# Kernel optimization log

Hardware: AMD Instinct MI355X
Metric: run time of the kernel (lower is better)

## Reference

```python
import jax, jax.numpy as jnp
import numpy as np

EPS = 1e-8
RESOLUTION = 32
DILATION = 1


def _stencils(resolution=RESOLUTION, dilation=DILATION):
    # interior grid of resolution^2 samples in [-1, 1]^2 (cell centers)
    lin = (np.arange(resolution) + 0.5) / resolution * 2.0 - 1.0
    gy, gx = np.meshgrid(lin, lin, indexing='ij')
    inner = np.stack([gy.ravel(), gx.ravel()], -1).astype(np.float32)
    # perimeter ring dilated outward by `dilation` cells
    scale = (resolution + 2.0 * dilation) / resolution
    mask = np.zeros((resolution, resolution), bool)
    mask[0, :] = mask[-1, :] = mask[:, 0] = mask[:, -1] = True
    outer = (inner[mask.ravel()] * scale).astype(np.float32)
    # append homogeneous coordinate (matches torch.concat with ones)
    s_in = np.concatenate([inner, np.ones((inner.shape[0], 1), np.float32)], -1)
    s_out = np.concatenate([outer, np.ones((outer.shape[0], 1), np.float32)], -1)
    return jnp.asarray(s_in), jnp.asarray(s_out)


def _bilinear(image, pos):
    # image: (H, W); pos: (..., 2) pixel coords (row, col); clamped bilinear
    H, W = image.shape
    i = pos[..., 0]
    j = pos[..., 1]
    i0 = jnp.clip(jnp.floor(i), 0, H - 2).astype(jnp.int32)
    j0 = jnp.clip(jnp.floor(j), 0, W - 2).astype(jnp.int32)
    di = jnp.clip(i - i0, 0.0, 1.0)
    dj = jnp.clip(j - j0, 0.0, 1.0)
    v00 = image[i0, j0]
    v01 = image[i0, j0 + 1]
    v10 = image[i0 + 1, j0]
    v11 = image[i0 + 1, j0 + 1]
    return (v00 * (1 - di) * (1 - dj) + v01 * (1 - di) * dj
            + v10 * di * (1 - dj) + v11 * di * dj)


def setup_inputs() -> dict:
    key = jax.random.key(0)
    k1, k2 = jax.random.split(key)
    S, P = 4, 4096
    H = W = 2048
    u = jax.random.uniform(k1, (S, P, 5), dtype=jnp.float32)
    xy = u[..., :2] * (H - 1)              # centers inside the image
    ab = 4.0 + u[..., 2:4] * 20.0          # half extents in [4, 24] px
    th = u[..., 4:5] * jnp.float32(np.pi)  # angle in [0, pi)
    points = jnp.concatenate([xy, ab, th], axis=-1)
    points_mask = jnp.ones((S, P), dtype=jnp.float32)
    position_energy_map = jax.random.normal(k2, (1, H, W), dtype=jnp.float32)
    stencil_in, stencil_out = _stencils()
    return {"points": points, "points_mask": points_mask,
            "position_energy_map": position_energy_map,
            "stencil_in": stencil_in, "stencil_out": stencil_out}


def reference(points, points_mask, position_energy_map, stencil_in, stencil_out):
    # affine_from_state: (x, y, a, b, theta) -> 2x3 affine, shape (S, P, 2, 3)
    x, y = points[..., 0], points[..., 1]
    a, b = points[..., 2], points[..., 3]
    t = points[..., 4]
    c, s = jnp.cos(t), jnp.sin(t)
    A = jnp.stack([jnp.stack([a * c, -b * s, x], -1),
                   jnp.stack([a * s, b * c, y], -1)], -2)
    # stencil coordinates in image space: (S, P, n_stencil, 2)
    coords_in = jnp.einsum('spij,nj->spni', A, stencil_in)
    coords_out = jnp.einsum('spij,nj->spni', A, stencil_out)
    img = position_energy_map[0]
    in_values = _bilinear(img, coords_in)    # (S, P, n_in)
    out_values = _bilinear(img, coords_out)  # (S, P, n_out)
    # contrast_measure: t-test-like contrast along stencil dim
    m_in, m_out = in_values.mean(-1), out_values.mean(-1)
    v_in = in_values.var(-1, ddof=1)
    v_out = out_values.var(-1, ddof=1)
    contrast = (m_in - m_out) / jnp.sqrt(v_in + v_out + EPS)
    return contrast * points_mask
```

## Files before the change

### kernel.cpp

```cpp
#include <hip/hip_runtime.h>
#include <math.h>

__global__ __launch_bounds__(256) void contrast_kernel_fast(
    const float* __restrict__ points,
    const float* __restrict__ mask,
    const float* __restrict__ img,
    float* __restrict__ out,
    int n_points)
{
    constexpr int W = 2048;
    constexpr int H = 2048;
    constexpr float fImax = (float)(H - 2);
    constexpr float fJmax = (float)(W - 2);

    const int wave = (int)((blockIdx.x * (unsigned)blockDim.x + threadIdx.x) >> 6);
    const int lane = (int)(threadIdx.x & 63u);
    if (wave >= n_points) return;

    const float* pt = points + (size_t)wave * 5;
    const float px = pt[0];
    const float py = pt[1];
    const float a  = pt[2];
    const float b  = pt[3];
    const float th = pt[4];

    float sn, cs;
    sincosf(th, &sn, &cs);
    const float A00 = a * cs, A01 = -b * sn;
    const float A10 = a * sn, A11 =  b * cs;

    const float sx = fmaf((float)(lane & 31), 0.0625f, 0.03125f) - 1.0f;
    const int   hi = lane >> 5;
    const float bi = fmaf(A01, sx, px);
    const float bj = fmaf(A11, sx, py);

    float s0 = 0.f, q0 = 0.f, s1 = 0.f, q1 = 0.f;
    #pragma unroll
    for (int it = 0; it < 16; ++it) {
        const float sy = fmaf((float)(2 * it + hi), 0.0625f, 0.03125f) - 1.0f;
        const float ci = fmaf(A00, sy, bi);
        const float cj = fmaf(A10, sy, bj);
        const float fi = fminf(fmaxf(floorf(ci), 0.f), fImax);
        const float fj = fminf(fmaxf(floorf(cj), 0.f), fJmax);
        const float di = fminf(fmaxf(ci - fi, 0.f), 1.f);
        const float dj = fminf(fmaxf(cj - fj, 0.f), 1.f);
        const float* p0 = img + (((int)fi << 11) + (int)fj);
        float2 r0, r1;
        __builtin_memcpy(&r0, p0, sizeof(float2));
        __builtin_memcpy(&r1, p0 + W, sizeof(float2));
        const float top = fmaf(r0.y - r0.x, dj, r0.x);
        const float bot = fmaf(r1.y - r1.x, dj, r1.x);
        const float v   = fmaf(bot - top, di, top);
        if (it & 1) { s1 += v; q1 = fmaf(v, v, q1); }
        else        { s0 += v; q0 = fmaf(v, v, q0); }
    }
    float sum_in = s0 + s1;
    float sq_in  = q0 + q1;

    float sum_out = 0.f, sq_out = 0.f;
    #pragma unroll
    for (int base = 0; base < 124; base += 64) {
        const int n = base + lane;
        if (n < 124) {
            int row, col;
            if (n < 32)      { row = 0;                 col = n; }
            else if (n < 92) { row = 1 + ((n - 32) >> 1); col = (n & 1) * 31; }
            else             { row = 31;                col = n - 92; }
            const float sy = (fmaf((float)row, 0.0625f, 0.03125f) - 1.0f) * 1.0625f;
            const float sxo = (fmaf((float)col, 0.0625f, 0.03125f) - 1.0f) * 1.0625f;
            const float ci = fmaf(A00, sy, fmaf(A01, sxo, px));
            const float cj = fmaf(A10, sy, fmaf(A11, sxo, py));
            const float fi = fminf(fmaxf(floorf(ci), 0.f), fImax);
            const float fj = fminf(fmaxf(floorf(cj), 0.f), fJmax);
            const float di = fminf(fmaxf(ci - fi, 0.f), 1.f);
            const float dj = fminf(fmaxf(cj - fj, 0.f), 1.f);
            const float* p0 = img + (((int)fi << 11) + (int)fj);
            float2 r0, r1;
            __builtin_memcpy(&r0, p0, sizeof(float2));
            __builtin_memcpy(&r1, p0 + W, sizeof(float2));
            const float top = fmaf(r0.y - r0.x, dj, r0.x);
            const float bot = fmaf(r1.y - r1.x, dj, r1.x);
            const float v   = fmaf(bot - top, di, top);
            sum_out += v;
            sq_out = fmaf(v, v, sq_out);
        }
    }

    #pragma unroll
    for (int off = 32; off > 0; off >>= 1) {
        sum_in  += __shfl_xor(sum_in,  off);
        sq_in   += __shfl_xor(sq_in,   off);
        sum_out += __shfl_xor(sum_out, off);
        sq_out  += __shfl_xor(sq_out,  off);
    }

    if (lane == 0) {
        const float ni = 1024.f, no = 124.f;
        const float m_in  = sum_in  / ni;
        const float m_out = sum_out / no;
        const float v_in  = (sq_in  - ni * m_in  * m_in ) / (ni - 1.f);
        const float v_out = (sq_out - no * m_out * m_out) / (no - 1.f);
        const float contrast = (m_in - m_out) / sqrtf(v_in + v_out + 1e-8f);
        out[wave] = contrast * mask[wave];
    }
}

__global__ __launch_bounds__(256) void contrast_kernel_generic(
    const float* __restrict__ points, const float* __restrict__ mask,
    const float* __restrict__ img, const float* __restrict__ st_in,
    const float* __restrict__ st_out, float* __restrict__ out,
    int n_points, int n_in, int n_out, int Himg, int Wimg)
{
    const int wave = (int)((blockIdx.x * (unsigned)blockDim.x + threadIdx.x) >> 6);
    const int lane = (int)(threadIdx.x & 63u);
    if (wave >= n_points) return;
    const float* pt = points + (size_t)wave * 5;
    const float px = pt[0], py = pt[1], a = pt[2], b = pt[3], th = pt[4];
    float sn, cs; sincosf(th, &sn, &cs);
    const float A00 = a * cs, A01 = -b * sn, A10 = a * sn, A11 = b * cs;
    const float fImax = (float)(Himg - 2), fJmax = (float)(Wimg - 2);
    float sum_in = 0.f, sq_in = 0.f;
    for (int base = 0; base < n_in; base += 64) {
        const int n = base + lane;
        if (n < n_in) {
            const float sy = st_in[n * 3 + 0], sx = st_in[n * 3 + 1];
            const float ci = fmaf(A00, sy, fmaf(A01, sx, px));
            const float cj = fmaf(A10, sy, fmaf(A11, sx, py));
            const float fi = fminf(fmaxf(floorf(ci), 0.f), fImax);
            const float fj = fminf(fmaxf(floorf(cj), 0.f), fJmax);
            const float di = fminf(fmaxf(ci - fi, 0.f), 1.f);
            const float dj = fminf(fmaxf(cj - fj, 0.f), 1.f);
            const float* p0 = img + ((int)fi * Wimg + (int)fj);
            const float v00 = p0[0], v01 = p0[1], v10 = p0[Wimg], v11 = p0[Wimg + 1];
            const float top = fmaf(v01 - v00, dj, v00);
            const float bot = fmaf(v11 - v10, dj, v10);
            const float v = fmaf(bot - top, di, top);
            sum_in += v; sq_in = fmaf(v, v, sq_in);
        }
    }
    float sum_out = 0.f, sq_out = 0.f;
    for (int base = 0; base < n_out; base += 64) {
        const int n = base + lane;
        if (n < n_out) {
            const float sy = st_out[n * 3 + 0], sx = st_out[n * 3 + 1];
            const float ci = fmaf(A00, sy, fmaf(A01, sx, px));
            const float cj = fmaf(A10, sy, fmaf(A11, sx, py));
            const float fi = fminf(fmaxf(floorf(ci), 0.f), fImax);
            const float fj = fminf(fmaxf(floorf(cj), 0.f), fJmax);
            const float di = fminf(fmaxf(ci - fi, 0.f), 1.f);
            const float dj = fminf(fmaxf(cj - fj, 0.f), 1.f);
            const float* p0 = img + ((int)fi * Wimg + (int)fj);
            const float v00 = p0[0], v01 = p0[1], v10 = p0[Wimg], v11 = p0[Wimg + 1];
            const float top = fmaf(v01 - v00, dj, v00);
            const float bot = fmaf(v11 - v10, dj, v10);
            const float v = fmaf(bot - top, di, top);
            sum_out += v; sq_out = fmaf(v, v, sq_out);
        }
    }
    #pragma unroll
    for (int off = 32; off > 0; off >>= 1) {
        sum_in += __shfl_xor(sum_in, off);  sq_in += __shfl_xor(sq_in, off);
        sum_out += __shfl_xor(sum_out, off); sq_out += __shfl_xor(sq_out, off);
    }
    if (lane == 0) {
        const float ni = (float)n_in, no = (float)n_out;
        const float m_in = sum_in / ni, m_out = sum_out / no;
        const float v_in = (sq_in - ni * m_in * m_in) / (ni - 1.f);
        const float v_out = (sq_out - no * m_out * m_out) / (no - 1.f);
        const float contrast = (m_in - m_out) / sqrtf(v_in + v_out + 1e-8f);
        out[wave] = contrast * mask[wave];
    }
}

extern "C" void kernel_launch(void* const* d_in, const int* in_sizes, int n_in_bufs,
                              void* d_out, int out_size, void* d_ws, size_t ws_size,
                              hipStream_t stream) {
    (void)n_in_bufs; (void)d_ws; (void)ws_size; (void)out_size;
    const float* points = (const float*)d_in[0];
    const float* mask   = (const float*)d_in[1];
    const float* img    = (const float*)d_in[2];
    const float* st_in  = (const float*)d_in[3];
    const float* st_out = (const float*)d_in[4];
    float* out = (float*)d_out;

    const int n_points = in_sizes[0] / 5;
    const int n_in     = in_sizes[3] / 3;
    const int n_out    = in_sizes[4] / 3;
    const int hw       = in_sizes[2];

    const int waves_per_block = 4;
    const int blocks = (n_points + waves_per_block - 1) / waves_per_block;

    if (n_in == 1024 && n_out == 124 && hw == 2048 * 2048) {
        contrast_kernel_fast<<<blocks, 256, 0, stream>>>(points, mask, img, out, n_points);
    } else {
        int Wimg = 1;
        while ((long long)Wimg * Wimg < (long long)hw) Wimg <<= 1;
        const int Himg = hw / Wimg;
        contrast_kernel_generic<<<blocks, 256, 0, stream>>>(points, mask, img, st_in, st_out,
                                                            out, n_points, n_in, n_out, Himg, Wimg);
    }
}
```

Measured before the change: 116.6 us.

## Split each point across two waves with 8x8 tiled stencil sampling

Each point is now handled by two waves in a block instead of one, so the block covers two points. Each wave samples half of the 1024 inner stencil points and half of the 124 outer ones, and the two partial sums are combined through shared memory after a __syncthreads. Inner samples are assigned in 8x8 spatial tiles rather than 32-wide rows, so the gather addresses of one instruction are more compact in the image. The aim is more waves in flight to hide gather latency and better cache-line reuse, at the cost of a block-level barrier and duplicated per-point setup such as sincos.

```diff
diff --git a/kernel.cpp b/kernel.cpp
--- a/kernel.cpp
+++ b/kernel.cpp
@@ -13,11 +13,15 @@
     constexpr float fImax = (float)(H - 2);
     constexpr float fJmax = (float)(W - 2);
 
-    const int wave = (int)((blockIdx.x * (unsigned)blockDim.x + threadIdx.x) >> 6);
+    __shared__ float partial[4][4];
+
+    const int wib  = (int)(threadIdx.x >> 6);
     const int lane = (int)(threadIdx.x & 63u);
-    if (wave >= n_points) return;
-
-    const float* pt = points + (size_t)wave * 5;
+    const int pid  = blockIdx.x * 2 + (wib >> 1);
+    const int half = wib & 1;
+    if (pid >= n_points) return;
+
+    const float* pt = points + (size_t)pid * 5;
     const float px = pt[0];
     const float py = pt[1];
     const float a  = pt[2];
@@ -29,17 +33,23 @@
     const float A00 = a * cs, A01 = -b * sn;
     const float A10 = a * sn, A11 =  b * cs;
 
-    const float sx = fmaf((float)(lane & 31), 0.0625f, 0.03125f) - 1.0f;
-    const int   hi = lane >> 5;
-    const float bi = fmaf(A01, sx, px);
-    const float bj = fmaf(A11, sx, py);
+    const int r8 = lane >> 3;
+    const int c8 = lane & 7;
+    const float sy0 = fmaf((float)r8, 0.0625f, 0.03125f) - 1.0f;
+    const float sx0 = fmaf((float)c8, 0.0625f, 0.03125f) - 1.0f;
+    const float ci0 = fmaf(A00, sy0, fmaf(A01, sx0, px));
+    const float cj0 = fmaf(A10, sy0, fmaf(A11, sx0, py));
+    const float A00h = A00 * 0.5f, A01h = A01 * 0.5f;
+    const float A10h = A10 * 0.5f, A11h = A11 * 0.5f;
 
     float s0 = 0.f, q0 = 0.f, s1 = 0.f, q1 = 0.f;
     #pragma unroll
-    for (int it = 0; it < 16; ++it) {
-        const float sy = fmaf((float)(2 * it + hi), 0.0625f, 0.03125f) - 1.0f;
-        const float ci = fmaf(A00, sy, bi);
-        const float cj = fmaf(A10, sy, bj);
+    for (int t = 0; t < 8; ++t) {
+        const int tile = half * 8 + t;
+        const float ftr = (float)(tile >> 2);
+        const float ftc = (float)(tile & 3);
+        const float ci = fmaf(A00h, ftr, fmaf(A01h, ftc, ci0));
+        const float cj = fmaf(A10h, ftr, fmaf(A11h, ftc, cj0));
         const float fi = fminf(fmaxf(floorf(ci), 0.f), fImax);
         const float fj = fminf(fmaxf(floorf(cj), 0.f), fJmax);
         const float di = fminf(fmaxf(ci - fi, 0.f), 1.f);
@@ -51,25 +61,24 @@
         const float top = fmaf(r0.y - r0.x, dj, r0.x);
         const float bot = fmaf(r1.y - r1.x, dj, r1.x);
         const float v   = fmaf(bot - top, di, top);
-        if (it & 1) { s1 += v; q1 = fmaf(v, v, q1); }
-        else        { s0 += v; q0 = fmaf(v, v, q0); }
+        if (t & 1) { s1 += v; q1 = fmaf(v, v, q1); }
+        else       { s0 += v; q0 = fmaf(v, v, q0); }
     }
     float sum_in = s0 + s1;
     float sq_in  = q0 + q1;
 
     float sum_out = 0.f, sq_out = 0.f;
-    #pragma unroll
-    for (int base = 0; base < 124; base += 64) {
-        const int n = base + lane;
-        if (n < 124) {
+    {
+        const int n = half * 62 + lane;
+        if (lane < 62) {
             int row, col;
-            if (n < 32)      { row = 0;                 col = n; }
+            if (n < 32)      { row = 0;                   col = n; }
             else if (n < 92) { row = 1 + ((n - 32) >> 1); col = (n & 1) * 31; }
-            else             { row = 31;                col = n - 92; }
+            else             { row = 31;                  col = n - 92; }
             const float sy = (fmaf((float)row, 0.0625f, 0.03125f) - 1.0f) * 1.0625f;
-            const float sxo = (fmaf((float)col, 0.0625f, 0.03125f) - 1.0f) * 1.0625f;
-            const float ci = fmaf(A00, sy, fmaf(A01, sxo, px));
-            const float cj = fmaf(A10, sy, fmaf(A11, sxo, py));
+            const float sx = (fmaf((float)col, 0.0625f, 0.03125f) - 1.0f) * 1.0625f;
+            const float ci = fmaf(A00, sy, fmaf(A01, sx, px));
+            const float cj = fmaf(A10, sy, fmaf(A11, sx, py));
             const float fi = fminf(fmaxf(floorf(ci), 0.f), fImax);
             const float fj = fminf(fmaxf(floorf(cj), 0.f), fJmax);
             const float di = fminf(fmaxf(ci - fi, 0.f), 1.f);
@@ -81,8 +90,8 @@
             const float top = fmaf(r0.y - r0.x, dj, r0.x);
             const float bot = fmaf(r1.y - r1.x, dj, r1.x);
             const float v   = fmaf(bot - top, di, top);
-            sum_out += v;
-            sq_out = fmaf(v, v, sq_out);
+            sum_out = v;
+            sq_out  = v * v;
         }
     }
 
@@ -95,13 +104,25 @@
     }
 
     if (lane == 0) {
+        partial[wib][0] = sum_in;
+        partial[wib][1] = sq_in;
+        partial[wib][2] = sum_out;
+        partial[wib][3] = sq_out;
+    }
+    __syncthreads();
+
+    if (lane == 0 && half == 0) {
+        const float S_in  = partial[wib][0] + partial[wib + 1][0];
+        const float Q_in  = partial[wib][1] + partial[wib + 1][1];
+        const float S_out = partial[wib][2] + partial[wib + 1][2];
+        const float Q_out = partial[wib][3] + partial[wib + 1][3];
         const float ni = 1024.f, no = 124.f;
-        const float m_in  = sum_in  / ni;
-        const float m_out = sum_out / no;
-        const float v_in  = (sq_in  - ni * m_in  * m_in ) / (ni - 1.f);
-        const float v_out = (sq_out - no * m_out * m_out) / (no - 1.f);
+        const float m_in  = S_in  / ni;
+        const float m_out = S_out / no;
+        const float v_in  = (Q_in  - ni * m_in  * m_in ) / (ni - 1.f);
+        const float v_out = (Q_out - no * m_out * m_out) / (no - 1.f);
         const float contrast = (m_in - m_out) / sqrtf(v_in + v_out + 1e-8f);
-        out[wave] = contrast * mask[wave];
+        out[pid] = contrast * mask[pid];
     }
 }
 
@@ -188,15 +209,14 @@
     const int n_out    = in_sizes[4] / 3;
     const int hw       = in_sizes[2];
 
-    const int waves_per_block = 4;
-    const int blocks = (n_points + waves_per_block - 1) / waves_per_block;
-
     if (n_in == 1024 && n_out == 124 && hw == 2048 * 2048) {
+        const int blocks = (n_points + 1) / 2;
         contrast_kernel_fast<<<blocks, 256, 0, stream>>>(points, mask, img, out, n_points);
     } else {
         int Wimg = 1;
         while ((long long)Wimg * Wimg < (long long)hw) Wimg <<= 1;
         const int Himg = hw / Wimg;
+        const int blocks = (n_points + 3) / 4;
         contrast_kernel_generic<<<blocks, 256, 0, stream>>>(points, mask, img, st_in, st_out,
                                                             out, n_points, n_in, n_out, Himg, Wimg);
     }
```

Result: no change. 118.7 us (+1.8%).

## Convert image to padded fp16 workspace and skip clamping for interior ellipses

Applied to the files above, without the earlier changes.

Adds a pre-pass that converts the fp32 energy map to fp16 with a padded row stride in the workspace, so the main kernel gathers half-size data with fewer cache misses. The main kernel picks an unclamped tap path when the ellipse's bounding box lies inside the image, and switches the inner loop from full unroll to unroll 2. The cost is an extra full-image conversion pass every call and fp16 rounding of the image values, which changes numerical accuracy.

```diff
diff --git a/kernel.cpp b/kernel.cpp
--- a/kernel.cpp
+++ b/kernel.cpp
@@ -1,18 +1,106 @@
 #include <hip/hip_runtime.h>
+#include <hip/hip_fp16.h>
 #include <math.h>
 
-__global__ __launch_bounds__(256) void contrast_kernel_fast(
+
+#define PSTRIDE 2080
+
+__global__ __launch_bounds__(256) void convert_img_f16_pad(
+    const float4* __restrict__ src, __half* __restrict__ dst)
+{
+    const int row = (int)blockIdx.x;
+    const int t   = (int)threadIdx.x;
+    const float4 a = src[(size_t)row * 512 + t * 2];
+    const float4 b = src[(size_t)row * 512 + t * 2 + 1];
+    union { __half2 h[4]; uint4 u; } o;
+    o.h[0] = __float22half2_rn(make_float2(a.x, a.y));
+    o.h[1] = __float22half2_rn(make_float2(a.z, a.w));
+    o.h[2] = __float22half2_rn(make_float2(b.x, b.y));
+    o.h[3] = __float22half2_rn(make_float2(b.z, b.w));
+    *(uint4*)(dst + (size_t)row * PSTRIDE + t * 8) = o.u;
+}
+
+template<bool CLAMP>
+__device__ __forceinline__ float tap_pad(const __half* __restrict__ img,
+                                         float ci, float cj)
+{
+    float fi = floorf(ci), fj = floorf(cj);
+    if (CLAMP) {
+        fi = fminf(fmaxf(fi, 0.f), 2046.f);
+        fj = fminf(fmaxf(fj, 0.f), 2046.f);
+    }
+    float di = ci - fi, dj = cj - fj;
+    if (CLAMP) {
+        di = fminf(fmaxf(di, 0.f), 1.f);
+        dj = fminf(fmaxf(dj, 0.f), 1.f);
+    }
+    const int r = (int)fi, c = (int)fj;
+    const int base = (r << 11) + (r << 5) + c;
+    const int even = base & ~1;
+    const int sh   = (base & 1) << 4;
+    uint2 q0, q1;
+    __builtin_memcpy(&q0, img + even, 8);
+    __builtin_memcpy(&q1, img + even + PSTRIDE, 8);
+    const unsigned p0 = (unsigned)((((unsigned long long)q0.y << 32) | q0.x) >> sh);
+    const unsigned p1 = (unsigned)((((unsigned long long)q1.y << 32) | q1.x) >> sh);
+    const float2 f0 = __half22float2(*reinterpret_cast<const __half2*>(&p0));
+    const float2 f1 = __half22float2(*reinterpret_cast<const __half2*>(&p1));
+    const float top = fmaf(f0.y - f0.x, dj, f0.x);
+    const float bot = fmaf(f1.y - f1.x, dj, f1.x);
+    return fmaf(bot - top, di, top);
+}
+
+template<bool CLAMP>
+__device__ __forceinline__ void accum_pad(
+    const __half* __restrict__ img, int lane,
+    float A00, float A01, float A10, float A11, float px, float py,
+    float& sum_in, float& sq_in, float& sum_out, float& sq_out)
+{
+    const float sx = fmaf((float)(lane & 31), 0.0625f, 0.03125f) - 1.0f;
+    const int   hi = lane >> 5;
+    const float bi = fmaf(A01, sx, px);
+    const float bj = fmaf(A11, sx, py);
+
+    float s0 = 0.f, q0 = 0.f, s1 = 0.f, q1 = 0.f;
+    #pragma unroll 2
+    for (int it = 0; it < 16; ++it) {
+        const float sy = fmaf((float)(2 * it + hi), 0.0625f, 0.03125f) - 1.0f;
+        const float ci = fmaf(A00, sy, bi);
+        const float cj = fmaf(A10, sy, bj);
+        const float v  = tap_pad<CLAMP>(img, ci, cj);
+        if (it & 1) { s1 += v; q1 = fmaf(v, v, q1); }
+        else        { s0 += v; q0 = fmaf(v, v, q0); }
+    }
+    sum_in = s0 + s1;
+    sq_in  = q0 + q1;
+
+    sum_out = 0.f; sq_out = 0.f;
+    #pragma unroll
+    for (int base = 0; base < 124; base += 64) {
+        const int n = base + lane;
+        if (n < 124) {
+            int row, col;
+            if (n < 32)      { row = 0;                   col = n; }
+            else if (n < 92) { row = 1 + ((n - 32) >> 1); col = (n & 1) * 31; }
+            else             { row = 31;                  col = n - 92; }
+            const float sy = (fmaf((float)row, 0.0625f, 0.03125f) - 1.0f) * 1.0625f;
+            const float sxo = (fmaf((float)col, 0.0625f, 0.03125f) - 1.0f) * 1.0625f;
+            const float ci = fmaf(A00, sy, fmaf(A01, sxo, px));
+            const float cj = fmaf(A10, sy, fmaf(A11, sxo, py));
+            const float v  = tap_pad<CLAMP>(img, ci, cj);
+            sum_out += v;
+            sq_out = fmaf(v, v, sq_out);
+        }
+    }
+}
+
+__global__ __launch_bounds__(256, 8) void contrast_f16_pad(
     const float* __restrict__ points,
     const float* __restrict__ mask,
-    const float* __restrict__ img,
+    const __half* __restrict__ img,
     float* __restrict__ out,
     int n_points)
 {
-    constexpr int W = 2048;
-    constexpr int H = 2048;
-    constexpr float fImax = (float)(H - 2);
-    constexpr float fJmax = (float)(W - 2);
-
     const int wave = (int)((blockIdx.x * (unsigned)blockDim.x + threadIdx.x) >> 6);
     const int lane = (int)(threadIdx.x & 63u);
     if (wave >= n_points) return;
@@ -29,13 +117,58 @@
     const float A00 = a * cs, A01 = -b * sn;
     const float A10 = a * sn, A11 =  b * cs;
 
+    const float Ri = (fabsf(A00) + fabsf(A01)) * 1.04f;
+    const float Rj = (fabsf(A10) + fabsf(A11)) * 1.04f;
+    const bool interior = (px >= Ri + 0.5f) && (px <= 2046.0f - Ri) &&
+                          (py >= Rj + 0.5f) && (py <= 2046.0f - Rj);
+
+    float sum_in, sq_in, sum_out, sq_out;
+    if (interior) {
+        accum_pad<false>(img, lane, A00, A01, A10, A11, px, py,
+                         sum_in, sq_in, sum_out, sq_out);
+    } else {
+        accum_pad<true>(img, lane, A00, A01, A10, A11, px, py,
+                        sum_in, sq_in, sum_out, sq_out);
+    }
+
+    #pragma unroll
+    for (int off = 32; off > 0; off >>= 1) {
+        sum_in  += __shfl_xor(sum_in,  off);
+        sq_in   += __shfl_xor(sq_in,   off);
+        sum_out += __shfl_xor(sum_out, off);
+        sq_out  += __shfl_xor(sq_out,  off);
+    }
+
+    if (lane == 0) {
+        const float ni = 1024.f, no = 124.f;
+        const float m_in  = sum_in  / ni;
+        const float m_out = sum_out / no;
+        const float v_in  = (sq_in  - ni * m_in  * m_in ) / (ni - 1.f);
+        const float v_out = (sq_out - no * m_out * m_out) / (no - 1.f);
+        const float contrast = (m_in - m_out) / sqrtf(v_in + v_out + 1e-8f);
+        out[wave] = contrast * mask[wave];
+    }
+}
+
+__global__ __launch_bounds__(256) void contrast_kernel_fast(
+    const float* __restrict__ points, const float* __restrict__ mask,
+    const float* __restrict__ img, float* __restrict__ out, int n_points)
+{
+    constexpr int W = 2048;
+    constexpr float fImax = 2046.f, fJmax = 2046.f;
+    const int wave = (int)((blockIdx.x * (unsigned)blockDim.x + threadIdx.x) >> 6);
+    const int lane = (int)(threadIdx.x & 63u);
+    if (wave >= n_points) return;
+    const float* pt = points + (size_t)wave * 5;
+    const float px = pt[0], py = pt[1], a = pt[2], b = pt[3], th = pt[4];
+    float sn, cs; sincosf(th, &sn, &cs);
+    const float A00 = a * cs, A01 = -b * sn, A10 = a * sn, A11 = b * cs;
     const float sx = fmaf((float)(lane & 31), 0.0625f, 0.03125f) - 1.0f;
-    const int   hi = lane >> 5;
+    const int hi = lane >> 5;
     const float bi = fmaf(A01, sx, px);
     const float bj = fmaf(A11, sx, py);
-
     float s0 = 0.f, q0 = 0.f, s1 = 0.f, q1 = 0.f;
-    #pragma unroll
+    #pragma unroll 2
     for (int it = 0; it < 16; ++it) {
         const float sy = fmaf((float)(2 * it + hi), 0.0625f, 0.03125f) - 1.0f;
         const float ci = fmaf(A00, sy, bi);
@@ -50,22 +183,20 @@
         __builtin_memcpy(&r1, p0 + W, sizeof(float2));
         const float top = fmaf(r0.y - r0.x, dj, r0.x);
         const float bot = fmaf(r1.y - r1.x, dj, r1.x);
-        const float v   = fmaf(bot - top, di, top);
+        const float v = fmaf(bot - top, di, top);
         if (it & 1) { s1 += v; q1 = fmaf(v, v, q1); }
         else        { s0 += v; q0 = fmaf(v, v, q0); }
     }
-    float sum_in = s0 + s1;
-    float sq_in  = q0 + q1;
-
+    float sum_in = s0 + s1, sq_in = q0 + q1;
     float sum_out = 0.f, sq_out = 0.f;
     #pragma unroll
     for (int base = 0; base < 124; base += 64) {
         const int n = base + lane;
         if (n < 124) {
             int row, col;
-            if (n < 32)      { row = 0;                 col = n; }
+            if (n < 32)      { row = 0;                   col = n; }
             else if (n < 92) { row = 1 + ((n - 32) >> 1); col = (n & 1) * 31; }
-            else             { row = 31;                col = n - 92; }
+            else             { row = 31;                  col = n - 92; }
             const float sy = (fmaf((float)row, 0.0625f, 0.03125f) - 1.0f) * 1.0625f;
             const float sxo = (fmaf((float)col, 0.0625f, 0.03125f) - 1.0f) * 1.0625f;
             const float ci = fmaf(A00, sy, fmaf(A01, sxo, px));
@@ -80,12 +211,10 @@
             __builtin_memcpy(&r1, p0 + W, sizeof(float2));
             const float top = fmaf(r0.y - r0.x, dj, r0.x);
             const float bot = fmaf(r1.y - r1.x, dj, r1.x);
-            const float v   = fmaf(bot - top, di, top);
-            sum_out += v;
-            sq_out = fmaf(v, v, sq_out);
+            const float v = fmaf(bot - top, di, top);
+            sum_out += v; sq_out = fmaf(v, v, sq_out);
         }
     }
-
     #pragma unroll
     for (int off = 32; off > 0; off >>= 1) {
         sum_in  += __shfl_xor(sum_in,  off);
@@ -93,11 +222,9 @@
         sum_out += __shfl_xor(sum_out, off);
         sq_out  += __shfl_xor(sq_out,  off);
     }
-
     if (lane == 0) {
         const float ni = 1024.f, no = 124.f;
-        const float m_in  = sum_in  / ni;
-        const float m_out = sum_out / no;
+        const float m_in = sum_in / ni, m_out = sum_out / no;
         const float v_in  = (sq_in  - ni * m_in  * m_in ) / (ni - 1.f);
         const float v_out = (sq_out - no * m_out * m_out) / (no - 1.f);
         const float contrast = (m_in - m_out) / sqrtf(v_in + v_out + 1e-8f);
@@ -175,7 +302,7 @@
 extern "C" void kernel_launch(void* const* d_in, const int* in_sizes, int n_in_bufs,
                               void* d_out, int out_size, void* d_ws, size_t ws_size,
                               hipStream_t stream) {
-    (void)n_in_bufs; (void)d_ws; (void)ws_size; (void)out_size;
+    (void)n_in_bufs; (void)out_size;
     const float* points = (const float*)d_in[0];
     const float* mask   = (const float*)d_in[1];
     const float* img    = (const float*)d_in[2];
@@ -188,16 +315,22 @@
     const int n_out    = in_sizes[4] / 3;
     const int hw       = in_sizes[2];
 
-    const int waves_per_block = 4;
-    const int blocks = (n_points + waves_per_block - 1) / waves_per_block;
-
-    if (n_in == 1024 && n_out == 124 && hw == 2048 * 2048) {
-        contrast_kernel_fast<<<blocks, 256, 0, stream>>>(points, mask, img, out, n_points);
+    const bool canonical = (n_in == 1024 && n_out == 124 && hw == 2048 * 2048);
+    const size_t pad_bytes = (size_t)2048 * PSTRIDE * sizeof(__half) + 64;
+
+    if (canonical && ws_size >= pad_bytes) {
+        __half* img16 = (__half*)d_ws;
+        convert_img_f16_pad<<<2048, 256, 0, stream>>>((const float4*)img, img16);
+        contrast_f16_pad<<<(n_points + 3) / 4, 256, 0, stream>>>(
+            points, mask, img16, out, n_points);
+    } else if (canonical) {
+        contrast_kernel_fast<<<(n_points + 3) / 4, 256, 0, stream>>>(
+            points, mask, img, out, n_points);
     } else {
         int Wimg = 1;
         while ((long long)Wimg * Wimg < (long long)hw) Wimg <<= 1;
         const int Himg = hw / Wimg;
-        contrast_kernel_generic<<<blocks, 256, 0, stream>>>(points, mask, img, st_in, st_out,
-                                                            out, n_points, n_in, n_out, Himg, Wimg);
-    }
-}
+        contrast_kernel_generic<<<(n_points + 3) / 4, 256, 0, stream>>>(
+            points, mask, img, st_in, st_out, out, n_points, n_in, n_out, Himg, Wimg);
+    }
+}
```

Result: no change. 117.7 us (+0.9%).
